# Kernel tuning notes

Measured on AMD Instinct MI355X. Metric: run time of the kernel, lower is better.

Reference implementation:

```python
import jax, jax.numpy as jnp
import numpy as np

B, I, H = 8192, 1024, 1024

def setup_inputs() -> dict:
    key = jax.random.key(0)
    ks = jax.random.split(key, 6)
    s_in = 1.0 / np.sqrt(I)
    s_h = 1.0 / np.sqrt(H)
    return {
        "x": jax.random.normal(ks[0], (B, I), jnp.float32),
        "h_prev": jax.random.normal(ks[1], (B, H), jnp.float32),
        "c_prev": jax.random.normal(ks[2], (B, H), jnp.float32),
        "Wx": jax.random.normal(ks[3], (4, H, I), jnp.float32) * s_in,   # gate order: input, forget, cell, output
        "Wh": jax.random.normal(ks[4], (4, H, H), jnp.float32) * s_h,
        "bh": jax.random.normal(ks[5], (4, H), jnp.float32) * s_h,
    }

def reference(x, h_prev, c_prev, Wx, Wh, bh):
    # Fused: 2 batched GEMMs for all 4 gates -> [B, 4, H]
    gates = (jnp.einsum('bi,ghi->bgh', x, Wx)
             + jnp.einsum('bk,ghk->bgh', h_prev, Wh)
             + bh[None, :, :])
    i = jax.nn.sigmoid(gates[:, 0])
    f = jax.nn.sigmoid(gates[:, 1])
    g = jnp.tanh(gates[:, 2])
    o = jax.nn.sigmoid(gates[:, 3])
    c_next = f * c_prev + i * g
    h_next = o * jnp.tanh(c_next)
    return (h_next, c_next)
```

## Files before the change

### kernel.cpp

```cpp
#include <hip/hip_runtime.h>
#include <hip/hip_bf16.h>
#include <stdint.h>

#define B_DIM 8192
#define I_DIM 1024
#define H_DIM 1024

typedef __attribute__((ext_vector_type(8))) short short8;
typedef __attribute__((ext_vector_type(4))) float f32x4;

static __device__ __forceinline__ short f2b(float f) {
    __bf16 h = (__bf16)f;
    return __builtin_bit_cast(short, h);
}

static __device__ __forceinline__ short8 pack8(float4 a, float4 b) {
    short8 s;
    s[0] = f2b(a.x); s[1] = f2b(a.y); s[2] = f2b(a.z); s[3] = f2b(a.w);
    s[4] = f2b(b.x); s[5] = f2b(b.y); s[6] = f2b(b.z); s[7] = f2b(b.w);
    return s;
}

static __device__ __forceinline__ float sigmoid_f(float x) {
    return 1.0f / (1.0f + __expf(-x));
}

static __device__ __forceinline__ float tanh_fast(float x) {
    x = fminf(fmaxf(x, -15.0f), 15.0f);
    float e = __expf(2.0f * x);
    return (e - 1.0f) / (e + 1.0f);
}

static __device__ __forceinline__ void load_lds16(const void* gptr, void* lptr) {
    __builtin_amdgcn_global_load_lds(
        (const __attribute__((address_space(1))) uint32_t*)gptr,
        (__attribute__((address_space(3))) uint32_t*)lptr, 16, 0, 0);
}

#define GA_GROUPS (512 * 32 * 2 * 64)
#define GB_GROUPS (256 * 32 * 2 * 64)

__global__ __launch_bounds__(256) void convert_kernel(
    const float* __restrict__ x, const float* __restrict__ h,
    const float* __restrict__ wx, const float* __restrict__ wh,
    short* __restrict__ Aw, short* __restrict__ Bw)
{
    const int64_t total = (int64_t)GA_GROUPS + GB_GROUPS;
    for (int64_t g = (int64_t)blockIdx.x * blockDim.x + threadIdx.x; g < total;
         g += (int64_t)gridDim.x * blockDim.x) {
        const float* src;
        short* dst;
        if (g < GA_GROUPS) {
            const int lane = (int)(g & 63);
            const int rest = (int)(g >> 6);
            const int kh   = rest & 1;
            const int tk   = (rest >> 1) & 31;
            const int mfrag = rest >> 6;
            const int row = (mfrag << 4) + (lane & 15);
            const int k   = (tk << 6) + (kh << 5) + ((lane >> 4) << 3);
            src = (k < 1024) ? (x + (size_t)row * 1024 + k)
                             : (h + (size_t)row * 1024 + (k - 1024));
            dst = Aw + (size_t)g * 8;
        } else {
            const int64_t gb = g - GA_GROUPS;
            const int lane = (int)(gb & 63);
            const int rest = (int)(gb >> 6);
            const int kh   = rest & 1;
            const int tk   = (rest >> 1) & 31;
            const int nfrag = rest >> 6;
            const int cf   = nfrag & 15;
            const int bn   = nfrag >> 4;
            const int gate = cf & 3;
            const int col  = (bn << 6) + ((cf >> 2) << 4) + (lane & 15);
            const int k    = (tk << 6) + (kh << 5) + ((lane >> 4) << 3);
            src = (k < 1024) ? (wx + ((size_t)(gate << 10) + col) * 1024 + k)
                             : (wh + ((size_t)(gate << 10) + col) * 1024 + (k - 1024));
            dst = Bw + (size_t)gb * 8;
        }
        float4 v0 = ((const float4*)src)[0];
        float4 v1 = ((const float4*)src)[1];
        *(short8*)dst = pack8(v0, v1);
    }
}

#define AOFF(d, f) ((d) * 8192 + (f) * 512)
#define BOFF(d, f) ((d) * 8192 + 4096 + (f) * 512)

__global__ __launch_bounds__(256, 3) void lstm_gemm_cnt_kernel(
    const short* __restrict__ Aw, const short* __restrict__ Bw,
    const float* __restrict__ cprev, const float* __restrict__ bh,
    float* __restrict__ out)
{
    __shared__ __align__(16) short smem[24576];

    const int bid = blockIdx.x;
    const int xcd = bid & 7;
    const int c   = bid >> 3;
    const int bm  = c >> 2;
    const int ht  = 4 * xcd + (c & 3);
    const int m0  = bm * 128;

    const int t    = threadIdx.x;
    const int lane = t & 63;
    const int w    = t >> 6;
    const int wm   = w >> 1;
    const int wn   = w & 1;
    const int lc   = lane & 15;

    const short* aSrc0 = Aw + (size_t)(bm * 8 + 2 * w)     * 32768 + lane * 8;
    const short* aSrc1 = Aw + (size_t)(bm * 8 + 2 * w + 1) * 32768 + lane * 8;
    const short* bSrc0 = Bw + (size_t)(ht * 8 + 2 * w)     * 32768 + lane * 8;
    const short* bSrc1 = Bw + (size_t)(ht * 8 + 2 * w + 1) * 32768 + lane * 8;

    f32x4 acc[4][4] = {};

#define STAGE(db, tp) \
    load_lds16(aSrc0 + (tp) * 512, &smem[AOFF(db, 2 * w)]); \
    load_lds16(aSrc1 + (tp) * 512, &smem[AOFF(db, 2 * w + 1)]); \
    load_lds16(bSrc0 + (tp) * 512, &smem[BOFF(db, 2 * w)]); \
    load_lds16(bSrc1 + (tp) * 512, &smem[BOFF(db, 2 * w + 1)]);

#define TILE(db, sdb, tp) do { \
    asm volatile("s_waitcnt vmcnt(4)" ::: "memory"); \
    __builtin_amdgcn_s_barrier(); \
    STAGE(sdb, tp) \
    short8 bv[4], av[4]; \
    _Pragma("unroll") \
    for (int j = 0; j < 4; ++j) \
        bv[j] = *(const short8*)&smem[BOFF(db, wn * 4 + j) + lane * 8]; \
    _Pragma("unroll") \
    for (int i = 0; i < 4; ++i) \
        av[i] = *(const short8*)&smem[AOFF(db, wm * 4 + i) + lane * 8]; \
    __builtin_amdgcn_s_setprio(1); \
    _Pragma("unroll") \
    for (int i = 0; i < 4; ++i) \
        _Pragma("unroll") \
        for (int j = 0; j < 4; ++j) \
            acc[i][j] = __builtin_amdgcn_mfma_f32_16x16x32_bf16( \
                av[i], bv[j], acc[i][j], 0, 0, 0); \
    __builtin_amdgcn_s_setprio(0); \
} while (0)

    STAGE(0, 0)
    STAGE(1, 1)

    #pragma unroll 1
    for (int tk3 = 0; tk3 < 21; ++tk3) {
        const int t0 = 3 * tk3;
        const int p2 = (t0 + 2 < 64) ? t0 + 2 : 63;
        const int p3 = (t0 + 3 < 64) ? t0 + 3 : 63;
        const int p4 = (t0 + 4 < 64) ? t0 + 4 : 63;
        TILE(0, 2, p2);
        TILE(1, 0, p3);
        TILE(2, 1, p4);
    }
    TILE(0, 2, 63);
#undef TILE
#undef STAGE
    asm volatile("s_waitcnt vmcnt(0)" ::: "memory");

    const int rg = lane >> 4;
    const int h  = ht * 32 + wn * 16 + lc;
    const float b_i = bh[0 * H_DIM + h];
    const float b_f = bh[1 * H_DIM + h];
    const float b_g = bh[2 * H_DIM + h];
    const float b_o = bh[3 * H_DIM + h];

    #pragma unroll
    for (int mf = 0; mf < 4; ++mf) {
        #pragma unroll
        for (int r = 0; r < 4; ++r) {
            const int row = m0 + wm * 64 + mf * 16 + rg * 4 + r;
            const float pi = acc[mf][0][r] + b_i;
            const float pf = acc[mf][1][r] + b_f;
            const float pg = acc[mf][2][r] + b_g;
            const float po = acc[mf][3][r] + b_o;
            const float iv = sigmoid_f(pi);
            const float fv = sigmoid_f(pf);
            const float gv = tanh_fast(pg);
            const float ov = sigmoid_f(po);
            const float cp = cprev[(size_t)row * H_DIM + h];
            const float cn = fv * cp + iv * gv;
            const float hn = ov * tanh_fast(cn);
            out[(size_t)row * H_DIM + h] = hn;
            out[(size_t)B_DIM * H_DIM + (size_t)row * H_DIM + h] = cn;
        }
    }
}

static __device__ __forceinline__ int swz(int row, int k) {
    int byte = (row << 7) + (k << 1);
    byte ^= (row & 7) << 4;
    return byte >> 1;
}

__global__ __launch_bounds__(256, 2) void lstm_fallback_kernel(
    const float* __restrict__ x, const float* __restrict__ hprev,
    const float* __restrict__ cprev, const float* __restrict__ Wx,
    const float* __restrict__ Wh, const float* __restrict__ bh,
    float* __restrict__ out)
{
    __shared__ __align__(16) short As[128 * 64];
    __shared__ __align__(16) short Bs[128 * 64];

    int bid = blockIdx.x;
    bid = (bid & 7) * 256 + (bid >> 3);
    const int mt = bid >> 5;
    const int ht = bid & 31;
    const int m0 = mt * 128;
    const int h0 = ht * 32;

    const int t    = threadIdx.x;
    const int lane = t & 63;
    const int w    = t >> 6;
    const int wr   = w >> 1;
    const int wc   = w & 1;

    const int srow = t >> 3;
    const int sk   = (t & 7) * 8;

    f32x4 acc[4][4] = {};

    #pragma unroll 1
    for (int phase = 0; phase < 2; ++phase) {
        const float* __restrict__ Ap = phase ? hprev : x;
        const float* __restrict__ Bp = phase ? Wh : Wx;
        #pragma unroll 1
        for (int kk = 0; kk < 1024; kk += 64) {
            __syncthreads();
            #pragma unroll
            for (int p = 0; p < 4; ++p) {
                const int row = srow + p * 32;
                const float4* src = (const float4*)(Ap + (size_t)(m0 + row) * I_DIM + kk + sk);
                *(short8*)&As[swz(row, sk)] = pack8(src[0], src[1]);
            }
            #pragma unroll
            for (int p = 0; p < 4; ++p) {
                const int n    = srow + p * 32;
                const int gate = (n >> 4) & 3;
                const int hcol = h0 + ((n >> 6) << 4) + (n & 15);
                const float4* src = (const float4*)(Bp + (size_t)((gate << 10) + hcol) * 1024 + kk + sk);
                *(short8*)&Bs[swz(n, sk)] = pack8(src[0], src[1]);
            }
            __syncthreads();
            #pragma unroll
            for (int ks = 0; ks < 2; ++ks) {
                const int kb = ks * 32 + ((lane >> 4) << 3);
                short8 a[4], b[4];
                #pragma unroll
                for (int m = 0; m < 4; ++m)
                    a[m] = *(const short8*)&As[swz(wr * 64 + m * 16 + (lane & 15), kb)];
                #pragma unroll
                for (int j = 0; j < 4; ++j)
                    b[j] = *(const short8*)&Bs[swz(wc * 64 + j * 16 + (lane & 15), kb)];
                #pragma unroll
                for (int m = 0; m < 4; ++m)
                    #pragma unroll
                    for (int j = 0; j < 4; ++j)
                        acc[m][j] = __builtin_amdgcn_mfma_f32_16x16x32_bf16(a[m], b[j], acc[m][j], 0, 0, 0);
            }
        }
    }

    const int cl = lane & 15;
    const int rg = lane >> 4;
    const int h  = h0 + wc * 16 + cl;
    const float b_i = bh[0 * H_DIM + h];
    const float b_f = bh[1 * H_DIM + h];
    const float b_g = bh[2 * H_DIM + h];
    const float b_o = bh[3 * H_DIM + h];

    #pragma unroll
    for (int m = 0; m < 4; ++m) {
        #pragma unroll
        for (int r = 0; r < 4; ++r) {
            const int row = m0 + wr * 64 + m * 16 + rg * 4 + r;
            const float pi = acc[m][0][r] + b_i;
            const float pf = acc[m][1][r] + b_f;
            const float pg = acc[m][2][r] + b_g;
            const float po = acc[m][3][r] + b_o;
            const float iv = sigmoid_f(pi);
            const float fv = sigmoid_f(pf);
            const float gv = tanh_fast(pg);
            const float ov = sigmoid_f(po);
            const float cp = cprev[(size_t)row * H_DIM + h];
            const float cn = fv * cp + iv * gv;
            const float hn = ov * tanh_fast(cn);
            out[(size_t)row * H_DIM + h] = hn;
            out[(size_t)B_DIM * H_DIM + (size_t)row * H_DIM + h] = cn;
        }
    }
}

extern "C" void kernel_launch(void* const* d_in, const int* in_sizes, int n_in,
                              void* d_out, int out_size, void* d_ws, size_t ws_size,
                              hipStream_t stream) {
    const float* x     = (const float*)d_in[0];
    const float* hprev = (const float*)d_in[1];
    const float* cprev = (const float*)d_in[2];
    const float* Wx    = (const float*)d_in[3];
    const float* Wh    = (const float*)d_in[4];
    const float* bh    = (const float*)d_in[5];
    float* out = (float*)d_out;

    const size_t need = ((size_t)B_DIM * 2048 + (size_t)4096 * 2048) * sizeof(short);
    if (ws_size >= need && d_ws != nullptr) {
        short* Aw = (short*)d_ws;
        short* Bw = Aw + (size_t)512 * 32768;
        hipLaunchKernelGGL(convert_kernel, dim3(4096), dim3(256), 0, stream,
                           x, hprev, Wx, Wh, Aw, Bw);
        hipLaunchKernelGGL(lstm_gemm_cnt_kernel, dim3(2048), dim3(256), 0, stream,
                           Aw, Bw, cprev, bh, out);
    } else {
        hipLaunchKernelGGL(lstm_fallback_kernel, dim3(2048), dim3(256), 0, stream,
                           x, hprev, cprev, Wx, Wh, bh, out);
    }
}
```

Baseline: 151.5 us.

## Enlarge GEMM block tile to 256 rows for more B-operand reuse

Doubles the M extent of each workgroup's tile from 128 to 256 rows, so every wave now holds 8x4 MFMA accumulators and each block stages six 16-byte loads per k-step into a larger triple-buffered LDS region (72 KB, dynamic). The grid halves to 1024 blocks and launch bounds drop to 2 waves-per-SIMD occupancy. The aim is to cut weight-tile reloads from global/L2 and raise the MFMA-to-LDS-read ratio. The cost is more register pressure, lower occupancy, and fewer blocks to balance across CUs.

```diff
diff --git a/kernel.cpp b/kernel.cpp
--- a/kernel.cpp
+++ b/kernel.cpp
@@ -83,22 +83,22 @@
     }
 }
 
-#define AOFF(d, f) ((d) * 8192 + (f) * 512)
-#define BOFF(d, f) ((d) * 8192 + 4096 + (f) * 512)
-
-__global__ __launch_bounds__(256, 3) void lstm_gemm_cnt_kernel(
+#define AOFF(d, f) ((d) * 12288 + (f) * 512)
+#define BOFF(d, f) ((d) * 12288 + 8192 + (f) * 512)
+
+__global__ __launch_bounds__(256, 2) void lstm_gemm_big_kernel(
     const short* __restrict__ Aw, const short* __restrict__ Bw,
     const float* __restrict__ cprev, const float* __restrict__ bh,
     float* __restrict__ out)
 {
-    __shared__ __align__(16) short smem[24576];
+    extern __shared__ __align__(16) short smem[];
 
     const int bid = blockIdx.x;
     const int xcd = bid & 7;
     const int c   = bid >> 3;
     const int bm  = c >> 2;
-    const int ht  = 4 * xcd + (c & 3);
-    const int m0  = bm * 128;
+    const int nt  = 4 * xcd + (c & 3);
+    const int m0  = bm * 256;
 
     const int t    = threadIdx.x;
     const int lane = t & 63;
@@ -107,37 +107,54 @@
     const int wn   = w & 1;
     const int lc   = lane & 15;
 
-    const short* aSrc0 = Aw + (size_t)(bm * 8 + 2 * w)     * 32768 + lane * 8;
-    const short* aSrc1 = Aw + (size_t)(bm * 8 + 2 * w + 1) * 32768 + lane * 8;
-    const short* bSrc0 = Bw + (size_t)(ht * 8 + 2 * w)     * 32768 + lane * 8;
-    const short* bSrc1 = Bw + (size_t)(ht * 8 + 2 * w + 1) * 32768 + lane * 8;
-
-    f32x4 acc[4][4] = {};
+    const short* aSrc0 = Aw + (size_t)(bm * 16 + 4 * w + 0) * 32768 + lane * 8;
+    const short* aSrc1 = Aw + (size_t)(bm * 16 + 4 * w + 1) * 32768 + lane * 8;
+    const short* aSrc2 = Aw + (size_t)(bm * 16 + 4 * w + 2) * 32768 + lane * 8;
+    const short* aSrc3 = Aw + (size_t)(bm * 16 + 4 * w + 3) * 32768 + lane * 8;
+    const short* bSrc0 = Bw + (size_t)(nt * 8 + 2 * w)     * 32768 + lane * 8;
+    const short* bSrc1 = Bw + (size_t)(nt * 8 + 2 * w + 1) * 32768 + lane * 8;
+
+    f32x4 acc[8][4] = {};
 
 #define STAGE(db, tp) \
-    load_lds16(aSrc0 + (tp) * 512, &smem[AOFF(db, 2 * w)]); \
-    load_lds16(aSrc1 + (tp) * 512, &smem[AOFF(db, 2 * w + 1)]); \
+    load_lds16(aSrc0 + (tp) * 512, &smem[AOFF(db, 4 * w + 0)]); \
+    load_lds16(aSrc1 + (tp) * 512, &smem[AOFF(db, 4 * w + 1)]); \
+    load_lds16(aSrc2 + (tp) * 512, &smem[AOFF(db, 4 * w + 2)]); \
+    load_lds16(aSrc3 + (tp) * 512, &smem[AOFF(db, 4 * w + 3)]); \
     load_lds16(bSrc0 + (tp) * 512, &smem[BOFF(db, 2 * w)]); \
     load_lds16(bSrc1 + (tp) * 512, &smem[BOFF(db, 2 * w + 1)]);
 
 #define TILE(db, sdb, tp) do { \
-    asm volatile("s_waitcnt vmcnt(4)" ::: "memory"); \
+    asm volatile("s_waitcnt vmcnt(6)" ::: "memory"); \
     __builtin_amdgcn_s_barrier(); \
     STAGE(sdb, tp) \
-    short8 bv[4], av[4]; \
+    short8 bv[4]; \
     _Pragma("unroll") \
     for (int j = 0; j < 4; ++j) \
         bv[j] = *(const short8*)&smem[BOFF(db, wn * 4 + j) + lane * 8]; \
+    short8 av0[4]; \
     _Pragma("unroll") \
     for (int i = 0; i < 4; ++i) \
-        av[i] = *(const short8*)&smem[AOFF(db, wm * 4 + i) + lane * 8]; \
+        av0[i] = *(const short8*)&smem[AOFF(db, wm * 8 + i) + lane * 8]; \
     __builtin_amdgcn_s_setprio(1); \
     _Pragma("unroll") \
     for (int i = 0; i < 4; ++i) \
         _Pragma("unroll") \
         for (int j = 0; j < 4; ++j) \
             acc[i][j] = __builtin_amdgcn_mfma_f32_16x16x32_bf16( \
-                av[i], bv[j], acc[i][j], 0, 0, 0); \
+                av0[i], bv[j], acc[i][j], 0, 0, 0); \
+    __builtin_amdgcn_s_setprio(0); \
+    short8 av1[4]; \
+    _Pragma("unroll") \
+    for (int i = 0; i < 4; ++i) \
+        av1[i] = *(const short8*)&smem[AOFF(db, wm * 8 + 4 + i) + lane * 8]; \
+    __builtin_amdgcn_s_setprio(1); \
+    _Pragma("unroll") \
+    for (int i = 0; i < 4; ++i) \
+        _Pragma("unroll") \
+        for (int j = 0; j < 4; ++j) \
+            acc[4 + i][j] = __builtin_amdgcn_mfma_f32_16x16x32_bf16( \
+                av1[i], bv[j], acc[4 + i][j], 0, 0, 0); \
     __builtin_amdgcn_s_setprio(0); \
 } while (0)
 
@@ -160,17 +177,17 @@
     asm volatile("s_waitcnt vmcnt(0)" ::: "memory");
 
     const int rg = lane >> 4;
-    const int h  = ht * 32 + wn * 16 + lc;
+    const int h  = nt * 32 + wn * 16 + lc;
     const float b_i = bh[0 * H_DIM + h];
     const float b_f = bh[1 * H_DIM + h];
     const float b_g = bh[2 * H_DIM + h];
     const float b_o = bh[3 * H_DIM + h];
 
     #pragma unroll
-    for (int mf = 0; mf < 4; ++mf) {
+    for (int mf = 0; mf < 8; ++mf) {
         #pragma unroll
         for (int r = 0; r < 4; ++r) {
-            const int row = m0 + wm * 64 + mf * 16 + rg * 4 + r;
+            const int row = m0 + wm * 128 + mf * 16 + rg * 4 + r;
             const float pi = acc[mf][0][r] + b_i;
             const float pf = acc[mf][1][r] + b_f;
             const float pg = acc[mf][2][r] + b_g;
@@ -305,11 +322,13 @@
 
     const size_t need = ((size_t)B_DIM * 2048 + (size_t)4096 * 2048) * sizeof(short);
     if (ws_size >= need && d_ws != nullptr) {
+        (void)hipFuncSetAttribute((const void*)lstm_gemm_big_kernel,
+                                  hipFuncAttributeMaxDynamicSharedMemorySize, 73728);
         short* Aw = (short*)d_ws;
         short* Bw = Aw + (size_t)512 * 32768;
         hipLaunchKernelGGL(convert_kernel, dim3(4096), dim3(256), 0, stream,
                            x, hprev, Wx, Wh, Aw, Bw);
-        hipLaunchKernelGGL(lstm_gemm_cnt_kernel, dim3(2048), dim3(256), 0, stream,
+        hipLaunchKernelGGL(lstm_gemm_big_kernel, dim3(1024), dim3(256), 73728, stream,
                            Aw, Bw, cprev, bh, out);
     } else {
         hipLaunchKernelGGL(lstm_fallback_kernel, dim3(2048), dim3(256), 0, stream,
```

After: 150.1 us. Within noise of the previous version (-0.9%).
